# Kernel optimization log

Measured on AMD Instinct MI355X. Metric: run time of the kernel, lower is better.

## Reference

```python
import jax, jax.numpy as jnp
import numpy as np

EPS = 1e-8  # torch CosineEmbeddingLoss default eps


def quat_to_mat(q):
    """(b,4) quaternion (w,x,y,z) -> (b,3,3) rotation matrix (normalized)."""
    q = q / jnp.clip(jnp.linalg.norm(q, axis=-1, keepdims=True), EPS)
    w, x, y, z = q[:, 0], q[:, 1], q[:, 2], q[:, 3]
    R = jnp.stack([
        jnp.stack([1 - 2 * (y * y + z * z), 2 * (x * y - w * z), 2 * (x * z + w * y)], axis=-1),
        jnp.stack([2 * (x * y + w * z), 1 - 2 * (x * x + z * z), 2 * (y * z - w * x)], axis=-1),
        jnp.stack([2 * (x * z - w * y), 2 * (y * z + w * x), 1 - 2 * (x * x + y * y)], axis=-1),
    ], axis=-2)  # (b,3,3)
    return R


def setup_inputs() -> dict:
    key = jax.random.key(0)
    k1, k2, k3 = jax.random.split(key, 3)
    return {
        "predquat": jax.random.normal(k1, (16, 4), dtype=jnp.float32),
        "gtquat": jax.random.normal(k2, (16, 4), dtype=jnp.float32),
        "points": jax.random.normal(k3, (16, 3, 2048), dtype=jnp.float32),
    }


def reference(predquat, gtquat, points):
    # CosineEmbeddingLoss with target=+1: mean(1 - cos_sim)
    dot = jnp.sum(predquat * gtquat, axis=-1)
    denom = jnp.clip(jnp.linalg.norm(predquat, axis=-1) * jnp.linalg.norm(gtquat, axis=-1), EPS)
    cos_loss = jnp.mean(1.0 - dot / denom)

    # rotate point clouds
    predrot = quat_to_mat(predquat)
    gtrot = quat_to_mat(gtquat)
    predpts = jnp.einsum('bij,bjn->bin', predrot, points)  # (b,3,np)
    gtpts = jnp.einsum('bij,bjn->bin', gtrot, points)      # (b,3,np)

    # chamfer/NN distance (original materializes (b,3,np,np); use cdist form)
    xsq = jnp.sum(gtpts ** 2, axis=1)                        # (b,np)
    ysq = jnp.sum(predpts ** 2, axis=1)                      # (b,np)
    cross = jnp.einsum('bcn,bcm->bnm', gtpts, predpts)       # (b,np,np)
    l2 = xsq[:, :, None] + ysq[:, None, :] - 2.0 * cross     # (b,np,np)
    min_l2 = jnp.min(l2, axis=1)                             # min over gt points, (b,np)
    pt_loss = jnp.mean(min_l2)
    pt_loss = jnp.where(jnp.isnan(pt_loss), jnp.zeros_like(pt_loss), pt_loss)

    # NOTE: the original torch module discards pt_loss and returns only cos_loss;
    # we return both so the dominant (chamfer) compute is observable.
    return cos_loss, pt_loss
```

## Files before the change

kernel.cpp:

```cpp
#include <hip/hip_runtime.h>
#include <math.h>

#define EPSF 1e-8f

constexpr int B = 16;
constexpr int N = 2048;
constexpr int NCHUNK = 4;
constexpr int MCHUNK = 4;
constexpr int NC = N / NCHUNK;
constexpr int MC = N / MCHUNK;
constexpr int THREADS = 256;

__device__ __forceinline__ void quat_to_mat(const float q[4], float R[3][3]) {
    float nrm = sqrtf(q[0]*q[0] + q[1]*q[1] + q[2]*q[2] + q[3]*q[3]);
    nrm = fmaxf(nrm, EPSF);
    float inv = 1.0f / nrm;
    float w = q[0]*inv, x = q[1]*inv, y = q[2]*inv, z = q[3]*inv;
    R[0][0] = 1.0f - 2.0f*(y*y + z*z);
    R[0][1] = 2.0f*(x*y - w*z);
    R[0][2] = 2.0f*(x*z + w*y);
    R[1][0] = 2.0f*(x*y + w*z);
    R[1][1] = 1.0f - 2.0f*(x*x + z*z);
    R[1][2] = 2.0f*(y*z - w*x);
    R[2][0] = 2.0f*(x*z - w*y);
    R[2][1] = 2.0f*(y*z + w*x);
    R[2][2] = 1.0f - 2.0f*(x*x + y*y);
}

__global__ __launch_bounds__(THREADS)
void quat_main_kernel(const float* __restrict__ predq,
                      const float* __restrict__ gtq,
                      const float* __restrict__ points,
                      float* __restrict__ partial,
                      float* __restrict__ out) {
    const int b  = blockIdx.x;
    const int mc = blockIdx.y;
    const int nc = blockIdx.z;
    const int t  = threadIdx.x;

    __shared__ float4 sp[NC];

    float pq[4], gq[4];
    #pragma unroll
    for (int i = 0; i < 4; ++i) { pq[i] = predq[4*b + i]; gq[i] = gtq[4*b + i]; }

    float Rp[3][3], Rg[3][3];
    quat_to_mat(pq, Rp);
    quat_to_mat(gq, Rg);

    float M[3][3];
    #pragma unroll
    for (int i = 0; i < 3; ++i)
        #pragma unroll
        for (int j = 0; j < 3; ++j) {
            float s = 0.0f;
            #pragma unroll
            for (int c = 0; c < 3; ++c) s = fmaf(Rg[c][i], Rp[c][j], s);
            M[i][j] = s;
        }

    if (mc == 0 && nc == 0 && t == 0) {
        float dot = pq[0]*gq[0] + pq[1]*gq[1] + pq[2]*gq[2] + pq[3]*gq[3];
        float np_ = sqrtf(pq[0]*pq[0] + pq[1]*pq[1] + pq[2]*pq[2] + pq[3]*pq[3]);
        float ng_ = sqrtf(gq[0]*gq[0] + gq[1]*gq[1] + gq[2]*gq[2] + gq[3]*gq[3]);
        float denom = fmaxf(np_ * ng_, EPSF);
        atomicAdd(out, (1.0f - dot / denom) * (1.0f / (float)B));
    }

    const float* P = points + (size_t)b * 3 * N;
    const int n0 = nc * NC;
    #pragma unroll
    for (int i = t; i < NC; i += THREADS) {
        float px = P[n0 + i];
        float py = P[N + n0 + i];
        float pz = P[2*N + n0 + i];
        sp[i] = make_float4(px, py, pz, fmaf(px, px, fmaf(py, py, pz*pz)));
    }
    __syncthreads();

    const int m1 = mc * MC + t;
    const int m2 = m1 + THREADS;

    float ax = P[m1], ay = P[N + m1], az = P[2*N + m1];
    float bx = P[m2], by = P[N + m2], bz = P[2*N + m2];

    float n1x = -2.0f * (M[0][0]*ax + M[0][1]*ay + M[0][2]*az);
    float n1y = -2.0f * (M[1][0]*ax + M[1][1]*ay + M[1][2]*az);
    float n1z = -2.0f * (M[2][0]*ax + M[2][1]*ay + M[2][2]*az);
    float n2x = -2.0f * (M[0][0]*bx + M[0][1]*by + M[0][2]*bz);
    float n2y = -2.0f * (M[1][0]*bx + M[1][1]*by + M[1][2]*bz);
    float n2z = -2.0f * (M[2][0]*bx + M[2][1]*by + M[2][2]*bz);

    float min1 = 3.4e38f, min2 = 3.4e38f;
    #pragma unroll 8
    for (int n = 0; n < NC; ++n) {
        float4 p = sp[n];
        float d1 = fmaf(p.x, n1x, p.w);
        d1 = fmaf(p.y, n1y, d1);
        d1 = fmaf(p.z, n1z, d1);
        min1 = fminf(min1, d1);
        float d2 = fmaf(p.x, n2x, p.w);
        d2 = fmaf(p.y, n2y, d2);
        d2 = fmaf(p.z, n2z, d2);
        min2 = fminf(min2, d2);
    }

    partial[(size_t)nc * B * N + (size_t)b * N + m1] = min1;
    partial[(size_t)nc * B * N + (size_t)b * N + m2] = min2;
}

__global__ __launch_bounds__(THREADS)
void quat_finalize_kernel(const float* __restrict__ points,
                          const float* __restrict__ partial,
                          float* __restrict__ out) {
    const int i = blockIdx.x * THREADS + threadIdx.x;
    const int b = i >> 11;
    const int m = i & (N - 1);

    float v0 = partial[i];
    float v1 = partial[B*N + i];
    float v2 = partial[2*B*N + i];
    float v3 = partial[3*B*N + i];
    float mn = fminf(fminf(v0, v1), fminf(v2, v3));

    const float* P = points + (size_t)b * 3 * N;
    float px = P[m], py = P[N + m], pz = P[2*N + m];
    float v = mn + fmaf(px, px, fmaf(py, py, pz*pz));

    #pragma unroll
    for (int o = 32; o > 0; o >>= 1) v += __shfl_down(v, o, 64);

    __shared__ float wsum[THREADS / 64];
    const int lane = threadIdx.x & 63;
    const int wid  = threadIdx.x >> 6;
    if (lane == 0) wsum[wid] = v;
    __syncthreads();
    if (threadIdx.x == 0) {
        float s = wsum[0] + wsum[1] + wsum[2] + wsum[3];
        atomicAdd(out + 1, s * (1.0f / (float)(B * N)));
    }
}

extern "C" void kernel_launch(void* const* d_in, const int* in_sizes, int n_in,
                              void* d_out, int out_size, void* d_ws, size_t ws_size,
                              hipStream_t stream) {
    const float* predq  = (const float*)d_in[0];
    const float* gtq    = (const float*)d_in[1];
    const float* points = (const float*)d_in[2];
    float* out = (float*)d_out;
    float* partial = (float*)d_ws;

    hipMemsetAsync(d_out, 0, 2 * sizeof(float), stream);

    dim3 grid(B, MCHUNK, NCHUNK);
    quat_main_kernel<<<grid, THREADS, 0, stream>>>(predq, gtq, points, partial, out);

    quat_finalize_kernel<<<B * N / THREADS, THREADS, 0, stream>>>(points, partial, out);
}
```

Before: 73.73 us.

## Split work per block over full N, reduce in-block, drop memset and atomics

The main kernel now gives each block 64 query points, with four waves each scanning a quarter of all 2048 reference points. The minima are combined in shared memory and summed to one partial per block, so only 512 floats are written instead of 4×B×N. The finalize kernel becomes a single block that also computes the cosine loss and writes the outputs directly, which removes the memset and the atomics. In exchange, each block loads all 2048 points into shared memory (32 KB), which may lower occupancy, and each thread keeps one running min instead of two, so there is less ILP.

```diff
diff --git a/kernel.cpp b/kernel.cpp
--- a/kernel.cpp
+++ b/kernel.cpp
@@ -5,11 +5,12 @@
 
 constexpr int B = 16;
 constexpr int N = 2048;
-constexpr int NCHUNK = 4;
-constexpr int MCHUNK = 4;
-constexpr int NC = N / NCHUNK;
-constexpr int MC = N / MCHUNK;
+constexpr int G = 32;
+constexpr int MB = N / G;
+constexpr int QS = 4;
+constexpr int NQ = N / QS;
 constexpr int THREADS = 256;
+constexpr int NPART = B * G;
 
 __device__ __forceinline__ void quat_to_mat(const float q[4], float R[3][3]) {
     float nrm = sqrtf(q[0]*q[0] + q[1]*q[1] + q[2]*q[2] + q[3]*q[3]);
@@ -31,23 +32,23 @@
 void quat_main_kernel(const float* __restrict__ predq,
                       const float* __restrict__ gtq,
                       const float* __restrict__ points,
-                      float* __restrict__ partial,
-                      float* __restrict__ out) {
-    const int b  = blockIdx.x;
-    const int mc = blockIdx.y;
-    const int nc = blockIdx.z;
-    const int t  = threadIdx.x;
+                      float* __restrict__ partial) {
+    const int b = blockIdx.x;
+    const int g = blockIdx.y;
+    const int t = threadIdx.x;
+    const int mi = t & (MB - 1);
+    const int q  = t >> 6;
 
-    __shared__ float4 sp[NC];
+    __shared__ float4 sp[N];
+    __shared__ float redmin[THREADS];
+    __shared__ float wsum;
 
     float pq[4], gq[4];
     #pragma unroll
     for (int i = 0; i < 4; ++i) { pq[i] = predq[4*b + i]; gq[i] = gtq[4*b + i]; }
-
     float Rp[3][3], Rg[3][3];
     quat_to_mat(pq, Rp);
     quat_to_mat(gq, Rg);
-
     float M[3][3];
     #pragma unroll
     for (int i = 0; i < 3; ++i)
@@ -59,85 +60,86 @@
             M[i][j] = s;
         }
 
-    if (mc == 0 && nc == 0 && t == 0) {
-        float dot = pq[0]*gq[0] + pq[1]*gq[1] + pq[2]*gq[2] + pq[3]*gq[3];
-        float np_ = sqrtf(pq[0]*pq[0] + pq[1]*pq[1] + pq[2]*pq[2] + pq[3]*pq[3]);
-        float ng_ = sqrtf(gq[0]*gq[0] + gq[1]*gq[1] + gq[2]*gq[2] + gq[3]*gq[3]);
-        float denom = fmaxf(np_ * ng_, EPSF);
-        atomicAdd(out, (1.0f - dot / denom) * (1.0f / (float)B));
-    }
-
     const float* P = points + (size_t)b * 3 * N;
-    const int n0 = nc * NC;
     #pragma unroll
-    for (int i = t; i < NC; i += THREADS) {
-        float px = P[n0 + i];
-        float py = P[N + n0 + i];
-        float pz = P[2*N + n0 + i];
+    for (int i = t; i < N; i += THREADS) {
+        float px = P[i];
+        float py = P[N + i];
+        float pz = P[2*N + i];
         sp[i] = make_float4(px, py, pz, fmaf(px, px, fmaf(py, py, pz*pz)));
     }
     __syncthreads();
 
-    const int m1 = mc * MC + t;
-    const int m2 = m1 + THREADS;
+    const int m = g * MB + mi;
+    const float ax = P[m], ay = P[N + m], az = P[2*N + m];
+    const float nx = -2.0f * (M[0][0]*ax + M[0][1]*ay + M[0][2]*az);
+    const float ny = -2.0f * (M[1][0]*ax + M[1][1]*ay + M[1][2]*az);
+    const float nz = -2.0f * (M[2][0]*ax + M[2][1]*ay + M[2][2]*az);
 
-    float ax = P[m1], ay = P[N + m1], az = P[2*N + m1];
-    float bx = P[m2], by = P[N + m2], bz = P[2*N + m2];
-
-    float n1x = -2.0f * (M[0][0]*ax + M[0][1]*ay + M[0][2]*az);
-    float n1y = -2.0f * (M[1][0]*ax + M[1][1]*ay + M[1][2]*az);
-    float n1z = -2.0f * (M[2][0]*ax + M[2][1]*ay + M[2][2]*az);
-    float n2x = -2.0f * (M[0][0]*bx + M[0][1]*by + M[0][2]*bz);
-    float n2y = -2.0f * (M[1][0]*bx + M[1][1]*by + M[1][2]*bz);
-    float n2z = -2.0f * (M[2][0]*bx + M[2][1]*by + M[2][2]*bz);
-
-    float min1 = 3.4e38f, min2 = 3.4e38f;
+    float mn = 3.4e38f;
+    const int n0 = q * NQ;
     #pragma unroll 8
-    for (int n = 0; n < NC; ++n) {
-        float4 p = sp[n];
-        float d1 = fmaf(p.x, n1x, p.w);
-        d1 = fmaf(p.y, n1y, d1);
-        d1 = fmaf(p.z, n1z, d1);
-        min1 = fminf(min1, d1);
-        float d2 = fmaf(p.x, n2x, p.w);
-        d2 = fmaf(p.y, n2y, d2);
-        d2 = fmaf(p.z, n2z, d2);
-        min2 = fminf(min2, d2);
+    for (int n = 0; n < NQ; ++n) {
+        float4 p = sp[n0 + n];
+        float d = fmaf(p.x, nx, p.w);
+        d = fmaf(p.y, ny, d);
+        d = fmaf(p.z, nz, d);
+        mn = fminf(mn, d);
     }
 
-    partial[(size_t)nc * B * N + (size_t)b * N + m1] = min1;
-    partial[(size_t)nc * B * N + (size_t)b * N + m2] = min2;
+    redmin[t] = mn;
+    __syncthreads();
+    if (t < MB) {
+        float v = fminf(fminf(redmin[t], redmin[t + 64]),
+                        fminf(redmin[t + 128], redmin[t + 192]));
+        v += fmaf(ax, ax, fmaf(ay, ay, az*az));
+        #pragma unroll
+        for (int o = 32; o > 0; o >>= 1) v += __shfl_down(v, o, 64);
+        if (t == 0) wsum = v;
+    }
+    __syncthreads();
+    if (t == 0) partial[b * G + g] = wsum;
 }
 
-__global__ __launch_bounds__(THREADS)
-void quat_finalize_kernel(const float* __restrict__ points,
+__global__ __launch_bounds__(NPART)
+void quat_finalize_kernel(const float* __restrict__ predq,
+                          const float* __restrict__ gtq,
                           const float* __restrict__ partial,
                           float* __restrict__ out) {
-    const int i = blockIdx.x * THREADS + threadIdx.x;
-    const int b = i >> 11;
-    const int m = i & (N - 1);
+    const int t = threadIdx.x;
+    const int lane = t & 63;
+    const int wid  = t >> 6;
 
-    float v0 = partial[i];
-    float v1 = partial[B*N + i];
-    float v2 = partial[2*B*N + i];
-    float v3 = partial[3*B*N + i];
-    float mn = fminf(fminf(v0, v1), fminf(v2, v3));
+    __shared__ float wpart[NPART / 64];
+    __shared__ float csum;
 
-    const float* P = points + (size_t)b * 3 * N;
-    float px = P[m], py = P[N + m], pz = P[2*N + m];
-    float v = mn + fmaf(px, px, fmaf(py, py, pz*pz));
-
+    float v = partial[t];
     #pragma unroll
     for (int o = 32; o > 0; o >>= 1) v += __shfl_down(v, o, 64);
+    if (lane == 0) wpart[wid] = v;
 
-    __shared__ float wsum[THREADS / 64];
-    const int lane = threadIdx.x & 63;
-    const int wid  = threadIdx.x >> 6;
-    if (lane == 0) wsum[wid] = v;
+    float c = 0.0f;
+    if (t < B) {
+        float pq0 = predq[4*t+0], pq1 = predq[4*t+1], pq2 = predq[4*t+2], pq3 = predq[4*t+3];
+        float gq0 = gtq[4*t+0],   gq1 = gtq[4*t+1],   gq2 = gtq[4*t+2],   gq3 = gtq[4*t+3];
+        float dot = pq0*gq0 + pq1*gq1 + pq2*gq2 + pq3*gq3;
+        float np_ = sqrtf(pq0*pq0 + pq1*pq1 + pq2*pq2 + pq3*pq3);
+        float ng_ = sqrtf(gq0*gq0 + gq1*gq1 + gq2*gq2 + gq3*gq3);
+        float denom = fmaxf(np_ * ng_, EPSF);
+        c = 1.0f - dot / denom;
+    }
+    if (wid == 0) {
+        #pragma unroll
+        for (int o = 8; o > 0; o >>= 1) c += __shfl_down(c, o, 64);
+        if (t == 0) csum = c;
+    }
     __syncthreads();
-    if (threadIdx.x == 0) {
-        float s = wsum[0] + wsum[1] + wsum[2] + wsum[3];
-        atomicAdd(out + 1, s * (1.0f / (float)(B * N)));
+    if (t == 0) {
+        float s = 0.0f;
+        #pragma unroll
+        for (int i = 0; i < NPART / 64; ++i) s += wpart[i];
+        out[0] = csum * (1.0f / (float)B);
+        out[1] = s * (1.0f / (float)(B * N));
     }
 }
 
@@ -150,10 +152,7 @@
     float* out = (float*)d_out;
     float* partial = (float*)d_ws;
 
-    hipMemsetAsync(d_out, 0, 2 * sizeof(float), stream);
-
-    dim3 grid(B, MCHUNK, NCHUNK);
-    quat_main_kernel<<<grid, THREADS, 0, stream>>>(predq, gtq, points, partial, out);
-
-    quat_finalize_kernel<<<B * N / THREADS, THREADS, 0, stream>>>(points, partial, out);
+    dim3 grid(B, G);
+    quat_main_kernel<<<grid, THREADS, 0, stream>>>(predq, gtq, points, partial);
+    quat_finalize_kernel<<<1, NPART, 0, stream>>>(predq, gtq, partial, out);
 }
```

New measurement: 95.02 us. +28.9%, slower.

## Register-block 8 queries per thread and split gt points into 32 chunks

Applied to the files above, without the earlier changes.

Each thread now keeps 8 query points in registers and scans a 64-point shared tile, so every LDS load of a gt point feeds 8 distance evaluations instead of 2. The grid becomes B x 32 chunks over the gt points, and the finalize kernel reduces 32 partial minima per query instead of 4. The memset is removed; the main kernel writes the cosine loss directly and zeroes the chamfer slot, which relies on that write happening before the finalize kernel's atomics. The trade is more partial-buffer traffic and higher register pressure per thread.

```diff
diff --git a/kernel.cpp b/kernel.cpp
--- a/kernel.cpp
+++ b/kernel.cpp
@@ -5,11 +5,10 @@
 
 constexpr int B = 16;
 constexpr int N = 2048;
-constexpr int NCHUNK = 4;
-constexpr int MCHUNK = 4;
-constexpr int NC = N / NCHUNK;
-constexpr int MC = N / MCHUNK;
+constexpr int NCH = 32;
+constexpr int NC = N / NCH;
 constexpr int THREADS = 256;
+constexpr int MPT = N / THREADS;
 
 __device__ __forceinline__ void quat_to_mat(const float q[4], float R[3][3]) {
     float nrm = sqrtf(q[0]*q[0] + q[1]*q[1] + q[2]*q[2] + q[3]*q[3]);
@@ -34,8 +33,7 @@
                       float* __restrict__ partial,
                       float* __restrict__ out) {
     const int b  = blockIdx.x;
-    const int mc = blockIdx.y;
-    const int nc = blockIdx.z;
+    const int nc = blockIdx.y;
     const int t  = threadIdx.x;
 
     __shared__ float4 sp[NC];
@@ -43,11 +41,9 @@
     float pq[4], gq[4];
     #pragma unroll
     for (int i = 0; i < 4; ++i) { pq[i] = predq[4*b + i]; gq[i] = gtq[4*b + i]; }
-
     float Rp[3][3], Rg[3][3];
     quat_to_mat(pq, Rp);
     quat_to_mat(gq, Rg);
-
     float M[3][3];
     #pragma unroll
     for (int i = 0; i < 3; ++i)
@@ -59,54 +55,56 @@
             M[i][j] = s;
         }
 
-    if (mc == 0 && nc == 0 && t == 0) {
-        float dot = pq[0]*gq[0] + pq[1]*gq[1] + pq[2]*gq[2] + pq[3]*gq[3];
-        float np_ = sqrtf(pq[0]*pq[0] + pq[1]*pq[1] + pq[2]*pq[2] + pq[3]*pq[3]);
-        float ng_ = sqrtf(gq[0]*gq[0] + gq[1]*gq[1] + gq[2]*gq[2] + gq[3]*gq[3]);
-        float denom = fmaxf(np_ * ng_, EPSF);
-        atomicAdd(out, (1.0f - dot / denom) * (1.0f / (float)B));
+    if (b == 0 && nc == 0 && t == 0) {
+        float c = 0.0f;
+        for (int bb = 0; bb < B; ++bb) {
+            float p0 = predq[4*bb+0], p1 = predq[4*bb+1], p2 = predq[4*bb+2], p3 = predq[4*bb+3];
+            float g0 = gtq[4*bb+0],   g1 = gtq[4*bb+1],   g2 = gtq[4*bb+2],   g3 = gtq[4*bb+3];
+            float dot = p0*g0 + p1*g1 + p2*g2 + p3*g3;
+            float np_ = sqrtf(p0*p0 + p1*p1 + p2*p2 + p3*p3);
+            float ng_ = sqrtf(g0*g0 + g1*g1 + g2*g2 + g3*g3);
+            c += 1.0f - dot / fmaxf(np_ * ng_, EPSF);
+        }
+        out[0] = c * (1.0f / (float)B);
+        out[1] = 0.0f;
     }
 
     const float* P = points + (size_t)b * 3 * N;
-    const int n0 = nc * NC;
-    #pragma unroll
-    for (int i = t; i < NC; i += THREADS) {
-        float px = P[n0 + i];
-        float py = P[N + n0 + i];
-        float pz = P[2*N + n0 + i];
-        sp[i] = make_float4(px, py, pz, fmaf(px, px, fmaf(py, py, pz*pz)));
+    if (t < NC) {
+        int i = nc * NC + t;
+        float px = P[i];
+        float py = P[N + i];
+        float pz = P[2*N + i];
+        sp[t] = make_float4(px, py, pz, fmaf(px, px, fmaf(py, py, pz*pz)));
     }
     __syncthreads();
 
-    const int m1 = mc * MC + t;
-    const int m2 = m1 + THREADS;
+    float nx[MPT], ny[MPT], nz[MPT], mn[MPT];
+    #pragma unroll
+    for (int k = 0; k < MPT; ++k) {
+        int m = k * THREADS + t;
+        float ax = P[m], ay = P[N + m], az = P[2*N + m];
+        nx[k] = -2.0f * (M[0][0]*ax + M[0][1]*ay + M[0][2]*az);
+        ny[k] = -2.0f * (M[1][0]*ax + M[1][1]*ay + M[1][2]*az);
+        nz[k] = -2.0f * (M[2][0]*ax + M[2][1]*ay + M[2][2]*az);
+        mn[k] = 3.4e38f;
+    }
 
-    float ax = P[m1], ay = P[N + m1], az = P[2*N + m1];
-    float bx = P[m2], by = P[N + m2], bz = P[2*N + m2];
-
-    float n1x = -2.0f * (M[0][0]*ax + M[0][1]*ay + M[0][2]*az);
-    float n1y = -2.0f * (M[1][0]*ax + M[1][1]*ay + M[1][2]*az);
-    float n1z = -2.0f * (M[2][0]*ax + M[2][1]*ay + M[2][2]*az);
-    float n2x = -2.0f * (M[0][0]*bx + M[0][1]*by + M[0][2]*bz);
-    float n2y = -2.0f * (M[1][0]*bx + M[1][1]*by + M[1][2]*bz);
-    float n2z = -2.0f * (M[2][0]*bx + M[2][1]*by + M[2][2]*bz);
-
-    float min1 = 3.4e38f, min2 = 3.4e38f;
-    #pragma unroll 8
+    #pragma unroll 2
     for (int n = 0; n < NC; ++n) {
         float4 p = sp[n];
-        float d1 = fmaf(p.x, n1x, p.w);
-        d1 = fmaf(p.y, n1y, d1);
-        d1 = fmaf(p.z, n1z, d1);
-        min1 = fminf(min1, d1);
-        float d2 = fmaf(p.x, n2x, p.w);
-        d2 = fmaf(p.y, n2y, d2);
-        d2 = fmaf(p.z, n2z, d2);
-        min2 = fminf(min2, d2);
+        #pragma unroll
+        for (int k = 0; k < MPT; ++k) {
+            float d = fmaf(p.x, nx[k], p.w);
+            d = fmaf(p.y, ny[k], d);
+            d = fmaf(p.z, nz[k], d);
+            mn[k] = fminf(mn[k], d);
+        }
     }
 
-    partial[(size_t)nc * B * N + (size_t)b * N + m1] = min1;
-    partial[(size_t)nc * B * N + (size_t)b * N + m2] = min2;
+    float* dst = partial + (size_t)nc * B * N + (size_t)b * N;
+    #pragma unroll
+    for (int k = 0; k < MPT; ++k) dst[k * THREADS + t] = mn[k];
 }
 
 __global__ __launch_bounds__(THREADS)
@@ -117,11 +115,9 @@
     const int b = i >> 11;
     const int m = i & (N - 1);
 
-    float v0 = partial[i];
-    float v1 = partial[B*N + i];
-    float v2 = partial[2*B*N + i];
-    float v3 = partial[3*B*N + i];
-    float mn = fminf(fminf(v0, v1), fminf(v2, v3));
+    float mn = partial[i];
+    #pragma unroll
+    for (int nc = 1; nc < NCH; ++nc) mn = fminf(mn, partial[(size_t)nc * B * N + i]);
 
     const float* P = points + (size_t)b * 3 * N;
     float px = P[m], py = P[N + m], pz = P[2*N + m];
@@ -150,10 +146,7 @@
     float* out = (float*)d_out;
     float* partial = (float*)d_ws;
 
-    hipMemsetAsync(d_out, 0, 2 * sizeof(float), stream);
-
-    dim3 grid(B, MCHUNK, NCHUNK);
+    dim3 grid(B, NCH);
     quat_main_kernel<<<grid, THREADS, 0, stream>>>(predq, gtq, points, partial, out);
-
     quat_finalize_kernel<<<B * N / THREADS, THREADS, 0, stream>>>(points, partial, out);
 }
```

Measured after the change: 70.18 us. 1.05x faster.
